# Optimization experiments

Measured on AMD Instinct MI355X. Metric: run time of the kernel, lower is better.

Reference implementation:

```python
import jax, jax.numpy as jnp
import numpy as np

B, S, HID = 2, 2048, 1024
NH = 16
HD = HID // NH  # 64
ROPE_BASE = 10000.0
NEG_INF = -1e9


def _rope_emb(seq_len):
    # emb = cat(sin, cos) over head_dim, shape [1, S, 1, HD]
    inv_freq = 1.0 / (ROPE_BASE ** (jnp.arange(0, HD, 2, dtype=jnp.float32) / HD))
    pos = jnp.arange(seq_len, dtype=jnp.float32)
    sincos = pos[:, None] * inv_freq[None, :]            # [S, HD/2]
    emb = jnp.concatenate([jnp.sin(sincos), jnp.cos(sincos)], axis=-1)  # [S, HD]
    return emb[None, :, None, :]


def _apply_rope(x, emb):
    # Faithful to the (quirky) torch code: cos = emb[..., 1::2], sin = emb[..., ::2]
    cos = emb[..., 1::2]
    sin = emb[..., ::2]
    xe = x[..., ::2]
    xo = x[..., 1::2]
    return jnp.concatenate([xe * cos - xo * sin, xe * sin + xo * cos], axis=-1)


def setup_inputs() -> dict:
    key = jax.random.key(0)
    ks = jax.random.split(key, 5)
    hidden_states = jax.random.normal(ks[0], (B, S, HID), dtype=jnp.float32)
    # causal additive mask, broadcast over batch/heads
    causal = jnp.tril(jnp.ones((S, S), dtype=bool))
    attention_mask = jnp.where(causal, 0.0, NEG_INF).astype(jnp.float32)[None, None]
    scale = 1.0 / np.sqrt(HID)
    w_q = jax.random.normal(ks[1], (HID, HID), dtype=jnp.float32) * scale
    w_k = jax.random.normal(ks[2], (HID, HID), dtype=jnp.float32) * scale
    w_v = jax.random.normal(ks[3], (HID, HID), dtype=jnp.float32) * scale
    w_o = jax.random.normal(ks[4], (HID, HID), dtype=jnp.float32) * scale
    return {"hidden_states": hidden_states, "attention_mask": attention_mask,
            "w_q": w_q, "w_k": w_k, "w_v": w_v, "w_o": w_o}


def reference(hidden_states, attention_mask, w_q, w_k, w_v, w_o):
    b, s, _ = hidden_states.shape
    # torch Linear: x @ W.T (W is [out, in])
    q = (hidden_states @ w_q.T).reshape(b, s, NH, HD)
    k = (hidden_states @ w_k.T).reshape(b, s, NH, HD)
    v = (hidden_states @ w_v.T).reshape(b, s, NH, HD)
    emb = _rope_emb(s)
    q = _apply_rope(q, emb)
    k = _apply_rope(k, emb)
    # [b, h, s, d]
    q = q.transpose(0, 2, 1, 3)
    k = k.transpose(0, 2, 1, 3)
    v = v.transpose(0, 2, 1, 3)
    scores = jnp.einsum('bhqd,bhkd->bhqk', q, k) / np.sqrt(HD)
    scores = scores + attention_mask
    attn = jax.nn.softmax(scores, axis=-1)
    out = jnp.einsum('bhqk,bhkd->bhqd', attn, v)
    out = out.transpose(0, 2, 1, 3).reshape(b, s, HID)
    return out @ w_o.T
```

## Files before the change

### kernel.cpp

```cpp
#include <hip/hip_runtime.h>
#include <hip/hip_bf16.h>
#include <math.h>

typedef unsigned short u16;
typedef unsigned int   u32;
typedef unsigned long long u64;
typedef __attribute__((ext_vector_type(8))) short bf16x8;
typedef __attribute__((ext_vector_type(4))) short bf16x4;
typedef __attribute__((ext_vector_type(4))) float f32x4;

#define B_   2
#define S_   2048
#define HID_ 1024
#define NH_  16
#define HD_  64
#define MR_  (B_*S_)

#define QSCALE 0.1803368801111137f
#define MBIAS 32.0f

__device__ __forceinline__ u16 f2bf(float f) {
  union { float f; u32 u; } x; x.f = f;
  u32 r = x.u + 0x7fffu + ((x.u >> 16) & 1u);
  return (u16)(r >> 16);
}
__device__ __forceinline__ void gload16(const void* g, void* l) {
  __builtin_amdgcn_global_load_lds(
      (const __attribute__((address_space(1))) u32*)g,
      (__attribute__((address_space(3))) u32*)l, 16, 0, 0);
}

__global__ void k_cvt_all(const float* __restrict__ hs, const float* __restrict__ wq,
                          const float* __restrict__ wk, const float* __restrict__ wv,
                          const float* __restrict__ wo, ushort4* __restrict__ dst) {
  int i = blockIdx.x * blockDim.x + threadIdx.x;
  const float4* src;
  int idx;
  if (i < 1048576) {
    src = (const float4*)hs; idx = i;
  } else {
    int j = i - 1048576;
    int w = j >> 18; idx = j & 262143;
    src = (const float4*)(w == 0 ? wq : w == 1 ? wk : w == 2 ? wv : wo);
  }
  float4 v = src[idx];
  ushort4 o;
  o.x = f2bf(v.x); o.y = f2bf(v.y); o.z = f2bf(v.z); o.w = f2bf(v.w);
  dst[i] = o;
}

__global__ void k_rope_table(float2* __restrict__ tab) {
  int t = blockIdx.x * blockDim.x + threadIdx.x;
  int p = t >> 5, j = t & 31;
  double fp = (double)p;
  double c, s;
  if (j < 16) {
    s = sin(fp * pow(10000.0, -(2.0 * j) / 32.0));
    c = sin(fp * pow(10000.0, -(2.0 * j + 1.0) / 32.0));
  } else {
    s = cos(fp * pow(10000.0, -(2.0 * j - 32.0) / 32.0));
    c = cos(fp * pow(10000.0, -(2.0 * j - 31.0) / 32.0));
  }
  tab[p * 32 + j] = make_float2((float)c, (float)s);
}

__global__ __launch_bounds__(512) void k_qkv(
    const u16* __restrict__ A,
    const u16* __restrict__ W0, const u16* __restrict__ W1, const u16* __restrict__ W2,
    u16* __restrict__ O0, u16* __restrict__ O1, u16* __restrict__ O2,
    const float2* __restrict__ tab) {
  __shared__ __align__(16) u16 Alds[2][256 * 64];
  __shared__ __align__(16) u16 Blds[2][256 * 64];

  int tid = threadIdx.x;
  int lane = tid & 63, wave = tid >> 6;
  int id = blockIdx.x;
  int g = id >> 3, x = id & 7;
  int mt = 2 * x + (g & 1);
  int nt = g >> 1;
  int m0 = mt * 256;
  int wi = nt >> 2;
  const u16* W = (wi == 0) ? W0 : (wi == 1 ? W1 : W2);
  int n0 = (nt & 3) * 256;
  int wm = wave >> 2, wn = wave & 3;
  int lg = lane >> 4, lr = lane & 15;

  f32x4 acc[8][4];
  const f32x4 vz = {0.f, 0.f, 0.f, 0.f};
#pragma unroll
  for (int i = 0; i < 8; ++i)
#pragma unroll
    for (int j = 0; j < 4; ++j) acc[i][j] = vz;

  auto SA = [&](int t_, int d_, int h_) {
#pragma unroll
    for (int it = 0; it < 2; ++it) {
      int c = it * 512 + tid;
      int row = c >> 3, sl = c & 7;
      int cw = sl ^ (row & 7);
      gload16(&A[(size_t)(m0 + h_ * 128 + row) * HID_ + t_ * 64 + cw * 8],
              &Alds[d_][(h_ * 1024 + it * 512 + wave * 64) * 8]);
    }
  };
  auto SB = [&](int t_, int d_, int h_) {
#pragma unroll
    for (int it = 0; it < 2; ++it) {
      int c = it * 512 + tid;
      int row = c >> 3, sl = c & 7;
      int cw = sl ^ (row & 7);
      gload16(&W[(size_t)(n0 + h_ * 128 + row) * HID_ + t_ * 64 + cw * 8],
              &Blds[d_][(h_ * 1024 + it * 512 + wave * 64) * 8]);
    }
  };

  SA(0, 0, 0); SB(0, 0, 0); SA(0, 0, 1); SB(0, 0, 1);

  for (int t = 0; t < 16; ++t) {
    int cur = t & 1, nxt = cur ^ 1;
    bool more = (t < 15);

    asm volatile("s_waitcnt vmcnt(0)" ::: "memory");
    __builtin_amdgcn_s_barrier();

    if (more) { SA(t + 1, nxt, 0); SB(t + 1, nxt, 0); }

    bf16x8 bfr[4], afr[4];
#pragma unroll
    for (int kk = 0; kk < 2; ++kk) {
#pragma unroll
      for (int ni = 0; ni < 4; ++ni) {
        int row = wn * 64 + ni * 16 + lr;
        int ci = (kk * 4 + lg) ^ (row & 7);
        bfr[ni] = *(const bf16x8*)&Blds[cur][row * 64 + ci * 8];
      }
#pragma unroll
      for (int mi = 0; mi < 4; ++mi) {
        int row = wm * 128 + mi * 16 + lr;
        int ci = (kk * 4 + lg) ^ (row & 7);
        afr[mi] = *(const bf16x8*)&Alds[cur][row * 64 + ci * 8];
      }
      __builtin_amdgcn_s_setprio(1);
#pragma unroll
      for (int mi = 0; mi < 4; ++mi)
#pragma unroll
        for (int ni = 0; ni < 4; ++ni)
          acc[mi][ni] = __builtin_amdgcn_mfma_f32_16x16x32_bf16(afr[mi], bfr[ni], acc[mi][ni], 0, 0, 0);
      __builtin_amdgcn_s_setprio(0);

      if (kk == 0 && more) { SA(t + 1, nxt, 1); SB(t + 1, nxt, 1); }

#pragma unroll
      for (int mi = 0; mi < 4; ++mi) {
        int row = wm * 128 + (mi + 4) * 16 + lr;
        int ci = (kk * 4 + lg) ^ (row & 7);
        afr[mi] = *(const bf16x8*)&Alds[cur][row * 64 + ci * 8];
      }
      __builtin_amdgcn_s_setprio(1);
#pragma unroll
      for (int mi = 0; mi < 4; ++mi)
#pragma unroll
        for (int ni = 0; ni < 4; ++ni)
          acc[mi + 4][ni] = __builtin_amdgcn_mfma_f32_16x16x32_bf16(afr[mi], bfr[ni], acc[mi + 4][ni], 0, 0, 0);
      __builtin_amdgcn_s_setprio(0);
    }
  }

  if (wi == 2) {
#pragma unroll
    for (int mi = 0; mi < 8; ++mi) {
      int grow0 = m0 + wm * 128 + mi * 16 + lg * 4;
      int bb = grow0 >> 11;
      int s = grow0 & 2047;
#pragma unroll
      for (int ni = 0; ni < 4; ++ni) {
        int gcol = n0 + wn * 64 + ni * 16 + lr;
        int h = gcol >> 6, dd = gcol & 63;
        u64 pk = (u64)f2bf(acc[mi][ni][0]) |
                 ((u64)f2bf(acc[mi][ni][1]) << 16) |
                 ((u64)f2bf(acc[mi][ni][2]) << 32) |
                 ((u64)f2bf(acc[mi][ni][3]) << 48);
        *(u64*)&O2[((size_t)(bb * NH_ + h) * HD_ + dd) * S_ + s] = pk;
      }
    }
  } else {
    u16* OB = wi ? O1 : O0;
    float sc = wi ? 1.0f : QSCALE;
#pragma unroll
    for (int mi = 0; mi < 8; ++mi) {
#pragma unroll
      for (int ni = 0; ni < 4; ++ni) {
        int gcol = n0 + wn * 64 + ni * 16 + lr;
        int h = gcol >> 6;
        int j = (gcol & 63) >> 1;
        bool even = !(gcol & 1);
        int ocol = h * 64 + (even ? j : 32 + j);
#pragma unroll
        for (int r = 0; r < 4; ++r) {
          float val = acc[mi][ni][r];
          float pv = __shfl_xor(val, 1);
          int grow = m0 + wm * 128 + mi * 16 + lg * 4 + r;
          int s = grow & 2047;
          float2 cs = tab[s * 32 + j];
          float xe = even ? val : pv;
          float xo = even ? pv : val;
          float res = even ? (xe * cs.x - xo * cs.y) : (xe * cs.y + xo * cs.x);
          OB[(size_t)grow * 1024 + ocol] = f2bf(res * sc);
        }
      }
    }
  }
}

__global__ __launch_bounds__(512) void k_oproj(
    const u16* __restrict__ A, const u16* __restrict__ W0,
    float* __restrict__ OF, int K) {
  __shared__ __align__(16) u16 Al[2][64 * 64];
  __shared__ __align__(16) u16 Bl[2][128 * 64];

  int tid = threadIdx.x;
  int lane = tid & 63, wave = tid >> 6;
  int m0 = blockIdx.y * 64;
  int n0 = blockIdx.x * 128;
  int wm = wave >> 1, wn = wave & 1;
  int lg = lane >> 4, lr = lane & 15;

  f32x4 acc[4];
  const f32x4 vz = {0.f, 0.f, 0.f, 0.f};
#pragma unroll
  for (int j = 0; j < 4; ++j) acc[j] = vz;

  auto STAGE = [&](int t_, int bs_) {
    int k0 = t_ * 64;
    {
      int c = tid;
      int row = c >> 3;
      int cw = (c & 7) ^ (row & 7);
      gload16(&A[(size_t)(m0 + row) * K + k0 + cw * 8], &Al[bs_][(wave * 64) * 8]);
    }
#pragma unroll
    for (int it = 0; it < 2; ++it) {
      int c = it * 512 + tid;
      int row = c >> 3;
      int cw = (c & 7) ^ (row & 7);
      gload16(&W0[(size_t)(n0 + row) * K + k0 + cw * 8], &Bl[bs_][(it * 512 + wave * 64) * 8]);
    }
  };

  int nkt = K >> 6;
  STAGE(0, 0);

  for (int t = 0; t < nkt; ++t) {
    int cur = t & 1;
    asm volatile("s_waitcnt vmcnt(0)" ::: "memory");
    __builtin_amdgcn_s_barrier();
    __builtin_amdgcn_sched_barrier(0);
    if (t + 1 < nkt) STAGE(t + 1, cur ^ 1);

#pragma unroll
    for (int kk = 0; kk < 2; ++kk) {
      bf16x8 af, bfr[4];
      {
        int row = wm * 16 + lr;
        int ci = (kk * 4 + lg) ^ (row & 7);
        af = *(const bf16x8*)&Al[cur][row * 64 + ci * 8];
      }
#pragma unroll
      for (int ni = 0; ni < 4; ++ni) {
        int row = wn * 64 + ni * 16 + lr;
        int ci = (kk * 4 + lg) ^ (row & 7);
        bfr[ni] = *(const bf16x8*)&Bl[cur][row * 64 + ci * 8];
      }
      __builtin_amdgcn_s_setprio(1);
#pragma unroll
      for (int ni = 0; ni < 4; ++ni)
        acc[ni] = __builtin_amdgcn_mfma_f32_16x16x32_bf16(af, bfr[ni], acc[ni], 0, 0, 0);
      __builtin_amdgcn_s_setprio(0);
    }
  }

#pragma unroll
  for (int ni = 0; ni < 4; ++ni)
#pragma unroll
    for (int r = 0; r < 4; ++r) {
      int grow = m0 + wm * 16 + lg * 4 + r;
      int gcol = n0 + wn * 64 + ni * 16 + lr;
      OF[(size_t)grow * 1024 + gcol] = acc[ni][r];
    }
}

__global__ __launch_bounds__(256, 4) void k_attn(
    const u16* __restrict__ Q, const u16* __restrict__ Kr, const u16* __restrict__ VT,
    u16* __restrict__ O) {
  __shared__ __align__(16) u16 Kl[2][64 * 64];
  __shared__ __align__(16) u16 Vl[2][64 * 64];

  int tid = threadIdx.x, lane = tid & 63, wave = tid >> 6;
  int id = blockIdx.x;
  int qt = 31 - (id >> 5);
  int bh = id & 31;
  int b = bh >> 4, h = bh & 15;
  int lg = lane >> 4, lr = lane & 15;
  int bS = b * S_;
  int nkt = qt + 1;
  int q0 = qt * 64 + wave * 16;

  const u16* vtb = &VT[(size_t)bh * HD_ * S_];
  int l8 = lane >> 3, l7 = lane & 7;
  int sl = l7 ^ l8;

  auto STAGE = [&](int kt_, int bs_) {
#pragma unroll
    for (int it = 0; it < 2; ++it) {
      int rb = wave * 16 + it * 8;
      int r = rb + l8;
      gload16(&Kr[(size_t)(bS + kt_ * 64 + r) * HID_ + h * HD_ + sl * 8],
              &Kl[bs_][rb * 64]);
      gload16(&vtb[(size_t)r * S_ + kt_ * 64 + sl * 8],
              &Vl[bs_][rb * 64]);
    }
  };

  STAGE(0, 0);

  bf16x8 qf[2];
#pragma unroll
  for (int kk = 0; kk < 2; ++kk)
    qf[kk] = *(const bf16x8*)
        &Q[(size_t)(bS + q0 + lr) * HID_ + h * HD_ + kk * 32 + lg * 8];

  f32x4 acc[4];
  const f32x4 vz = {0.f, 0.f, 0.f, 0.f};
#pragma unroll
  for (int df = 0; df < 4; ++df) acc[df] = vz;
  float l_ = 0.f;

  for (int kt = 0; kt < nkt; ++kt) {
    int cur = kt & 1;
    if (kt + 1 < nkt) {
      STAGE(kt + 1, cur ^ 1);
      asm volatile("s_waitcnt vmcnt(4)" ::: "memory");
    } else {
      asm volatile("s_waitcnt vmcnt(0)" ::: "memory");
    }
    __builtin_amdgcn_s_barrier();
    __builtin_amdgcn_sched_barrier(0);

    bf16x8 kfr[4][2];
#pragma unroll
    for (int kf = 0; kf < 4; ++kf) {
      int row = kf * 16 + lr;
#pragma unroll
      for (int kk = 0; kk < 2; ++kk) {
        int ci = (kk * 4 + lg) ^ (row & 7);
        kfr[kf][kk] = *(const bf16x8*)&Kl[cur][row * 64 + ci * 8];
      }
    }

    f32x4 st[4];
#pragma unroll
    for (int kf = 0; kf < 4; ++kf) st[kf] = vz;
    __builtin_amdgcn_s_setprio(1);
#pragma unroll
    for (int kk = 0; kk < 2; ++kk)
#pragma unroll
      for (int kf = 0; kf < 4; ++kf)
        st[kf] = __builtin_amdgcn_mfma_f32_16x16x32_bf16(
            kfr[kf][kk], qf[kk], st[kf], 0, 0, 0);
    __builtin_amdgcn_s_setprio(0);

    if (kt == qt) {
      int qg = q0 + lr;
#pragma unroll
      for (int kf = 0; kf < 4; ++kf)
#pragma unroll
        for (int r = 0; r < 4; ++r) {
          int kg = kt * 64 + kf * 16 + lg * 4 + r;
          if (kg > qg) st[kf][r] = -1e30f;
        }
    }

    float ts = 0.f;
    bf16x4 pb[4];
#pragma unroll
    for (int kf = 0; kf < 4; ++kf) {
#pragma unroll
      for (int r = 0; r < 4; ++r) {
        float e = __builtin_amdgcn_exp2f(st[kf][r] - MBIAS);
        st[kf][r] = e;
        ts += e;
      }
      u32 w0, w1;
      asm("v_cvt_pk_bf16_f32 %0, %1, %2" : "=v"(w0) : "v"(st[kf][0]), "v"(st[kf][1]));
      asm("v_cvt_pk_bf16_f32 %0, %1, %2" : "=v"(w1) : "v"(st[kf][2]), "v"(st[kf][3]));
      union { u32 u[2]; bf16x4 v; } pk;
      pk.u[0] = w0; pk.u[1] = w1;
      pb[kf] = pk.v;
    }
    l_ += ts;

    __builtin_amdgcn_s_setprio(1);
#pragma unroll
    for (int df = 0; df < 4; ++df) {
      int row = df * 16 + lr;
#pragma unroll
      for (int kf = 0; kf < 4; ++kf) {
        int slot = (kf * 2 + (lg >> 1)) ^ (row & 7);
        bf16x4 vfr = *(const bf16x4*)&Vl[cur][row * 64 + slot * 8 + (lg & 1) * 4];
        acc[df] = __builtin_amdgcn_mfma_f32_16x16x16bf16_1k(
            vfr, pb[kf], acc[df], 0, 0, 0);
      }
    }
    __builtin_amdgcn_s_setprio(0);

    __builtin_amdgcn_sched_barrier(0);
    __builtin_amdgcn_s_barrier();
  }

  l_ += __shfl_xor(l_, 16);
  l_ += __shfl_xor(l_, 32);
  float inv = 1.0f / l_;
  int grow = bS + q0 + lr;
#pragma unroll
  for (int df = 0; df < 4; ++df) {
    u64 pk = (u64)f2bf(acc[df][0] * inv) |
             ((u64)f2bf(acc[df][1] * inv) << 16) |
             ((u64)f2bf(acc[df][2] * inv) << 32) |
             ((u64)f2bf(acc[df][3] * inv) << 48);
    *(u64*)&O[(size_t)grow * HID_ + h * HD_ + df * 16 + lg * 4] = pk;
  }
}

extern "C" void kernel_launch(void* const* d_in, const int* in_sizes, int n_in,
                              void* d_out, int out_size, void* d_ws, size_t ws_size,
                              hipStream_t stream) {
  const float* hs = (const float*)d_in[0];
  const float* wq = (const float*)d_in[2];
  const float* wk = (const float*)d_in[3];
  const float* wv = (const float*)d_in[4];
  const float* wo = (const float*)d_in[5];
  float* out = (float*)d_out;

  char* ws = (char*)d_ws;
  const size_t P = (size_t)MR_ * HID_ * 2;
  u16* Xb  = (u16*)(ws);
  u16* Wqb = (u16*)(ws + P);
  u16* Wkb = (u16*)(ws + P + (size_t)HID_ * HID_ * 2);
  u16* Wvb = (u16*)(ws + P + (size_t)HID_ * HID_ * 4);
  u16* Wob = (u16*)(ws + P + (size_t)HID_ * HID_ * 6);
  u16* q_r = (u16*)(ws + 2 * P);
  u16* k_r = (u16*)(ws + 3 * P);
  u16* vt  = (u16*)(ws + 4 * P);
  float2* tab = (float2*)(ws + 5 * P);
  u16* attn_o = Xb;

  k_cvt_all<<<8192, 256, 0, stream>>>(hs, wq, wk, wv, wo, (ushort4*)ws);
  k_rope_table<<<256, 256, 0, stream>>>(tab);

  k_qkv<<<192, 512, 0, stream>>>(Xb, Wqb, Wkb, Wvb, q_r, k_r, vt, tab);

  k_attn<<<1024, 256, 0, stream>>>(q_r, k_r, vt, attn_o);

  k_oproj<<<dim3(8, 64), 512, 0, stream>>>(attn_o, Wob, out, HID_);
}
```

Baseline: 118.5 us.

## Retile fused QKV GEMM to 256x192 tiles over concatenated weights

```diff
diff --git a/kernel.cpp b/kernel.cpp
--- a/kernel.cpp
+++ b/kernel.cpp
@@ -65,135 +65,136 @@
 }
 
 __global__ __launch_bounds__(512) void k_qkv(
-    const u16* __restrict__ A,
-    const u16* __restrict__ W0, const u16* __restrict__ W1, const u16* __restrict__ W2,
-    u16* __restrict__ O0, u16* __restrict__ O1, u16* __restrict__ O2,
+    const u16* __restrict__ A, const u16* __restrict__ W,
+    u16* __restrict__ Oq, u16* __restrict__ Ok, u16* __restrict__ Ov,
     const float2* __restrict__ tab) {
-  __shared__ __align__(16) u16 Alds[2][256 * 64];
-  __shared__ __align__(16) u16 Blds[2][256 * 64];
+  __shared__ __align__(16) u16 Alds[2][2][256 * 32];
+  __shared__ __align__(16) u16 Blds[2][192 * 64];
 
   int tid = threadIdx.x;
   int lane = tid & 63, wave = tid >> 6;
   int id = blockIdx.x;
-  int g = id >> 3, x = id & 7;
+  int x = id & 7, g = id >> 3;
   int mt = 2 * x + (g & 1);
   int nt = g >> 1;
   int m0 = mt * 256;
-  int wi = nt >> 2;
-  const u16* W = (wi == 0) ? W0 : (wi == 1 ? W1 : W2);
-  int n0 = (nt & 3) * 256;
+  int n0 = nt * 192;
   int wm = wave >> 2, wn = wave & 3;
   int lg = lane >> 4, lr = lane & 15;
 
-  f32x4 acc[8][4];
+  f32x4 acc[8][3];
   const f32x4 vz = {0.f, 0.f, 0.f, 0.f};
 #pragma unroll
   for (int i = 0; i < 8; ++i)
 #pragma unroll
-    for (int j = 0; j < 4; ++j) acc[i][j] = vz;
-
-  auto SA = [&](int t_, int d_, int h_) {
-#pragma unroll
-    for (int it = 0; it < 2; ++it) {
+    for (int j = 0; j < 3; ++j) acc[i][j] = vz;
+
+  auto SB = [&](int t_, int d_) {
+#pragma unroll
+    for (int it = 0; it < 3; ++it) {
       int c = it * 512 + tid;
       int row = c >> 3, sl = c & 7;
       int cw = sl ^ (row & 7);
-      gload16(&A[(size_t)(m0 + h_ * 128 + row) * HID_ + t_ * 64 + cw * 8],
-              &Alds[d_][(h_ * 1024 + it * 512 + wave * 64) * 8]);
+      gload16(&W[(size_t)(n0 + row) * HID_ + t_ * 64 + cw * 8],
+              &Blds[d_][(it * 512 + wave * 64) * 8]);
     }
   };
-  auto SB = [&](int t_, int d_, int h_) {
+  auto SA = [&](int t_, int d_, int hk_) {
 #pragma unroll
     for (int it = 0; it < 2; ++it) {
       int c = it * 512 + tid;
-      int row = c >> 3, sl = c & 7;
-      int cw = sl ^ (row & 7);
-      gload16(&W[(size_t)(n0 + h_ * 128 + row) * HID_ + t_ * 64 + cw * 8],
-              &Blds[d_][(h_ * 1024 + it * 512 + wave * 64) * 8]);
+      int row = c >> 2, sl = c & 3;
+      int cw = sl ^ ((row >> 1) & 3);
+      gload16(&A[(size_t)(m0 + row) * HID_ + t_ * 64 + hk_ * 32 + cw * 8],
+              &Alds[d_][hk_][(it * 512 + wave * 64) * 8]);
     }
   };
 
-  SA(0, 0, 0); SB(0, 0, 0); SA(0, 0, 1); SB(0, 0, 1);
+  SB(0, 0); SA(0, 0, 0); SA(0, 0, 1);
 
   for (int t = 0; t < 16; ++t) {
     int cur = t & 1, nxt = cur ^ 1;
     bool more = (t < 15);
-
-    asm volatile("s_waitcnt vmcnt(0)" ::: "memory");
+    bf16x8 bfr[3], afr[8];
+
+    asm volatile("s_waitcnt vmcnt(2)" ::: "memory");
     __builtin_amdgcn_s_barrier();
-
-    if (more) { SA(t + 1, nxt, 0); SB(t + 1, nxt, 0); }
-
-    bf16x8 bfr[4], afr[4];
-#pragma unroll
-    for (int kk = 0; kk < 2; ++kk) {
-#pragma unroll
-      for (int ni = 0; ni < 4; ++ni) {
-        int row = wn * 64 + ni * 16 + lr;
-        int ci = (kk * 4 + lg) ^ (row & 7);
-        bfr[ni] = *(const bf16x8*)&Blds[cur][row * 64 + ci * 8];
-      }
-#pragma unroll
-      for (int mi = 0; mi < 4; ++mi) {
-        int row = wm * 128 + mi * 16 + lr;
-        int ci = (kk * 4 + lg) ^ (row & 7);
-        afr[mi] = *(const bf16x8*)&Alds[cur][row * 64 + ci * 8];
-      }
-      __builtin_amdgcn_s_setprio(1);
-#pragma unroll
-      for (int mi = 0; mi < 4; ++mi)
-#pragma unroll
-        for (int ni = 0; ni < 4; ++ni)
-          acc[mi][ni] = __builtin_amdgcn_mfma_f32_16x16x32_bf16(afr[mi], bfr[ni], acc[mi][ni], 0, 0, 0);
-      __builtin_amdgcn_s_setprio(0);
-
-      if (kk == 0 && more) { SA(t + 1, nxt, 1); SB(t + 1, nxt, 1); }
-
-#pragma unroll
-      for (int mi = 0; mi < 4; ++mi) {
-        int row = wm * 128 + (mi + 4) * 16 + lr;
-        int ci = (kk * 4 + lg) ^ (row & 7);
-        afr[mi] = *(const bf16x8*)&Alds[cur][row * 64 + ci * 8];
-      }
-      __builtin_amdgcn_s_setprio(1);
-#pragma unroll
-      for (int mi = 0; mi < 4; ++mi)
-#pragma unroll
-        for (int ni = 0; ni < 4; ++ni)
-          acc[mi + 4][ni] = __builtin_amdgcn_mfma_f32_16x16x32_bf16(afr[mi], bfr[ni], acc[mi + 4][ni], 0, 0, 0);
-      __builtin_amdgcn_s_setprio(0);
-    }
-  }
-
-  if (wi == 2) {
+    __builtin_amdgcn_sched_barrier(0);
+    if (more) { SB(t + 1, nxt); SA(t + 1, nxt, 0); }
+#pragma unroll
+    for (int ni = 0; ni < 3; ++ni) {
+      int row = wn * 48 + ni * 16 + lr;
+      int ci = lg ^ (row & 7);
+      bfr[ni] = *(const bf16x8*)&Blds[cur][row * 64 + ci * 8];
+    }
 #pragma unroll
     for (int mi = 0; mi < 8; ++mi) {
-      int grow0 = m0 + wm * 128 + mi * 16 + lg * 4;
-      int bb = grow0 >> 11;
-      int s = grow0 & 2047;
-#pragma unroll
-      for (int ni = 0; ni < 4; ++ni) {
-        int gcol = n0 + wn * 64 + ni * 16 + lr;
-        int h = gcol >> 6, dd = gcol & 63;
+      int row = wm * 128 + mi * 16 + lr;
+      int ci = lg ^ ((row >> 1) & 3);
+      afr[mi] = *(const bf16x8*)&Alds[cur][0][row * 32 + ci * 8];
+    }
+    __builtin_amdgcn_s_setprio(1);
+#pragma unroll
+    for (int mi = 0; mi < 8; ++mi)
+#pragma unroll
+      for (int ni = 0; ni < 3; ++ni)
+        acc[mi][ni] = __builtin_amdgcn_mfma_f32_16x16x32_bf16(afr[mi], bfr[ni], acc[mi][ni], 0, 0, 0);
+    __builtin_amdgcn_s_setprio(0);
+
+    if (more) { asm volatile("s_waitcnt vmcnt(5)" ::: "memory"); }
+    else      { asm volatile("s_waitcnt vmcnt(0)" ::: "memory"); }
+    __builtin_amdgcn_s_barrier();
+    __builtin_amdgcn_sched_barrier(0);
+    if (more) SA(t + 1, nxt, 1);
+#pragma unroll
+    for (int ni = 0; ni < 3; ++ni) {
+      int row = wn * 48 + ni * 16 + lr;
+      int ci = (4 + lg) ^ (row & 7);
+      bfr[ni] = *(const bf16x8*)&Blds[cur][row * 64 + ci * 8];
+    }
+#pragma unroll
+    for (int mi = 0; mi < 8; ++mi) {
+      int row = wm * 128 + mi * 16 + lr;
+      int ci = lg ^ ((row >> 1) & 3);
+      afr[mi] = *(const bf16x8*)&Alds[cur][1][row * 32 + ci * 8];
+    }
+    __builtin_amdgcn_s_setprio(1);
+#pragma unroll
+    for (int mi = 0; mi < 8; ++mi)
+#pragma unroll
+      for (int ni = 0; ni < 3; ++ni)
+        acc[mi][ni] = __builtin_amdgcn_mfma_f32_16x16x32_bf16(afr[mi], bfr[ni], acc[mi][ni], 0, 0, 0);
+    __builtin_amdgcn_s_setprio(0);
+  }
+
+#pragma unroll
+  for (int ni = 0; ni < 3; ++ni) {
+    int gcol = n0 + wn * 48 + ni * 16 + lr;
+    int wi = gcol >> 10;
+    if (wi == 2) {
+      int vcol = gcol & 1023;
+      int h = vcol >> 6, dd = vcol & 63;
+#pragma unroll
+      for (int mi = 0; mi < 8; ++mi) {
+        int grow0 = m0 + wm * 128 + mi * 16 + lg * 4;
+        int bb = grow0 >> 11;
+        int s = grow0 & 2047;
         u64 pk = (u64)f2bf(acc[mi][ni][0]) |
                  ((u64)f2bf(acc[mi][ni][1]) << 16) |
                  ((u64)f2bf(acc[mi][ni][2]) << 32) |
                  ((u64)f2bf(acc[mi][ni][3]) << 48);
-        *(u64*)&O2[((size_t)(bb * NH_ + h) * HD_ + dd) * S_ + s] = pk;
-      }
-    }
-  } else {
-    u16* OB = wi ? O1 : O0;
-    float sc = wi ? 1.0f : QSCALE;
-#pragma unroll
-    for (int mi = 0; mi < 8; ++mi) {
-#pragma unroll
-      for (int ni = 0; ni < 4; ++ni) {
-        int gcol = n0 + wn * 64 + ni * 16 + lr;
-        int h = gcol >> 6;
-        int j = (gcol & 63) >> 1;
-        bool even = !(gcol & 1);
-        int ocol = h * 64 + (even ? j : 32 + j);
+        *(u64*)&Ov[((size_t)(bb * NH_ + h) * HD_ + dd) * S_ + s] = pk;
+      }
+    } else {
+      u16* OB = wi ? Ok : Oq;
+      float sc = wi ? 1.0f : QSCALE;
+      int col = gcol & 1023;
+      int h = col >> 6;
+      int j = (col & 63) >> 1;
+      bool even = !(gcol & 1);
+      int ocol = h * 64 + (even ? j : 32 + j);
+#pragma unroll
+      for (int mi = 0; mi < 8; ++mi) {
 #pragma unroll
         for (int r = 0; r < 4; ++r) {
           float val = acc[mi][ni][r];
@@ -443,9 +444,7 @@
   char* ws = (char*)d_ws;
   const size_t P = (size_t)MR_ * HID_ * 2;
   u16* Xb  = (u16*)(ws);
-  u16* Wqb = (u16*)(ws + P);
-  u16* Wkb = (u16*)(ws + P + (size_t)HID_ * HID_ * 2);
-  u16* Wvb = (u16*)(ws + P + (size_t)HID_ * HID_ * 4);
+  u16* Wcat = (u16*)(ws + P);
   u16* Wob = (u16*)(ws + P + (size_t)HID_ * HID_ * 6);
   u16* q_r = (u16*)(ws + 2 * P);
   u16* k_r = (u16*)(ws + 3 * P);
@@ -456,7 +455,7 @@
   k_cvt_all<<<8192, 256, 0, stream>>>(hs, wq, wk, wv, wo, (ushort4*)ws);
   k_rope_table<<<256, 256, 0, stream>>>(tab);
 
-  k_qkv<<<192, 512, 0, stream>>>(Xb, Wqb, Wkb, Wvb, q_r, k_r, vt, tab);
+  k_qkv<<<256, 512, 0, stream>>>(Xb, Wcat, q_r, k_r, vt, tab);
 
   k_attn<<<1024, 256, 0, stream>>>(q_r, k_r, vt, attn_o);
 
```

Result: faster. 111.5 us (-5.9%).
